# Kernel optimization log

Hardware: AMD Instinct MI355X
Metric: run time of the kernel (lower is better)

Reference implementation:

```python
import jax, jax.numpy as jnp
import numpy as np

B, N, F, E, C, FC = 16, 5000, 512, 160000, 64, 128


def gcn_conv(x, src, dst, W, b, n_total):
    loop = jnp.arange(n_total, dtype=src.dtype)
    s = jnp.concatenate([src, loop])
    d = jnp.concatenate([dst, loop])
    deg = jax.ops.segment_sum(jnp.ones_like(s, dtype=x.dtype), d, num_segments=n_total)
    dinv = jnp.where(deg > 0, jax.lax.rsqrt(deg), 0.0)
    norm = dinv[s] * dinv[d]                      # [E']
    h = x @ W                                      # [n_total, out]
    msg = h[s] * norm[:, None]
    out = jax.ops.segment_sum(msg, d, num_segments=n_total)
    return out + b


def setup_inputs() -> dict:
    key = jax.random.key(0)
    ks = jax.random.split(key, 12)
    inp = {
        "node_features": jax.random.normal(ks[0], (B, N, F), jnp.float32),
        "col_features": jax.random.normal(ks[1], (B, C, FC), jnp.float32),
        "edge_index": jax.random.randint(ks[2], (2, E), 0, N, dtype=jnp.int64),
        # GCNConv 1/2 weights + node head
        "W1": jax.random.normal(ks[3], (F, 16), jnp.float32) / np.sqrt(F),
        "b1": jnp.zeros((16,), jnp.float32),
        "W2": jax.random.normal(ks[4], (16, 16), jnp.float32) / 4.0,
        "b2": jnp.zeros((16,), jnp.float32),
        "fc_w": jax.random.normal(ks[5], (16, 1), jnp.float32) / 4.0,
        "fc_b": jnp.zeros((1,), jnp.float32),
        # column MLP: Linear(FC,16) -> ReLU -> Linear(16,1)
        "cw1": jax.random.normal(ks[6], (FC, 16), jnp.float32) / np.sqrt(FC),
        "cb1": jnp.zeros((16,), jnp.float32),
        "cw2": jax.random.normal(ks[7], (16, 1), jnp.float32) / 4.0,
        "cb2": jnp.zeros((1,), jnp.float32),
    }
    return inp


def reference(node_features, col_features, edge_index, W1, b1, W2, b2, fc_w, fc_b, cw1, cb1, cw2, cb2):
    b, n, _ = node_features.shape
    n_total = b * n
    # batched edge_index via node-offset trick (shared graph per batch element)
    offsets = (jnp.arange(b, dtype=edge_index.dtype) * n)[:, None]   # [B,1]
    src = (edge_index[0][None, :] + offsets).reshape(-1)              # [B*E]
    dst = (edge_index[1][None, :] + offsets).reshape(-1)

    x = node_features.reshape(n_total, -1)
    x = jax.nn.relu(gcn_conv(x, src, dst, W1, b1, n_total))
    x = jax.nn.relu(gcn_conv(x, src, dst, W2, b2, n_total))
    node_logits = (x.reshape(b, n, 16) @ fc_w + fc_b)[..., 0]         # [B,N]

    h = jax.nn.relu(col_features @ cw1 + cb1)
    col_logits = (h @ cw2 + cb2)[..., 0]                              # [B,C]

    joint = node_logits[:, :, None] + col_logits[:, None, :]          # [B,N,C]
    return joint.reshape(b, -1)                                       # [B, N*C]
```

## Files before the change

kernel.cpp:

```cpp
#include <hip/hip_runtime.h>
#include <hip/hip_bf16.h>

typedef unsigned short u16;
typedef unsigned int   u32;

#define B_  16
#define N_  5000
#define F_  512
#define C_  64
#define FC_ 128
#define NT  (B_ * N_)

__device__ __forceinline__ float bf2f(u16 h) {
    return __uint_as_float(((u32)h) << 16);
}
__device__ __forceinline__ u16 f2bf(float f) {
    union { __hip_bfloat16 h; u16 s; } c; c.h = __float2bfloat16(f); return c.s;
}
__device__ __forceinline__ float ldw(const void* p, int i, int fF) {
    return fF ? bf2f(((const u16*)p)[i]) : ((const float*)p)[i];
}

__global__ __launch_bounds__(256) void det_k(const u32* __restrict__ x32,
                                             const u32* __restrict__ ei32,
                                             int* __restrict__ flags)
{
    __shared__ int cnt;
    __shared__ int orv;
    if (threadIdx.x == 0) { cnt = 0; orv = 0; }
    __syncthreads();
    u32 w = x32[threadIdx.x];
    int e = (int)((w >> 7) & 0xffu);
    if (e >= 112 && e <= 136) atomicAdd(&cnt, 1);
    if (threadIdx.x < 32) {
        if (ei32[2 * threadIdx.x + 1] != 0u) atomicOr(&orv, 1);
    }
    __syncthreads();
    if (threadIdx.x == 0) {
        flags[0] = (cnt >= 128) ? 1 : 0;
        flags[1] = (orv == 0) ? 1 : 0;
    }
}

__device__ __forceinline__ int src_at(const u32* ei32, int t, int E, int fI) {
    return (int)(fI ? ei32[2 * t] : ei32[t]);
}
__device__ __forceinline__ int dst_at(const u32* ei32, int t, int E, int fI) {
    return (int)(fI ? ei32[2 * (E + t)] : ei32[E + t]);
}

__global__ __launch_bounds__(256) void prep_weights(
    const void* __restrict__ W1, const void* __restrict__ W2,
    const void* __restrict__ fcw, const void* __restrict__ cw1,
    const void* __restrict__ cw2, const void* __restrict__ b1,
    const void* __restrict__ b2, const void* __restrict__ fcb,
    const void* __restrict__ cb1, const void* __restrict__ cb2,
    const int* __restrict__ flags,
    float* __restrict__ w1f, float* __restrict__ w2f, float* __restrict__ fcwf,
    float* __restrict__ cw1f, float* __restrict__ cw2f, float* __restrict__ b1f,
    float* __restrict__ b2f, float* __restrict__ fcbf, float* __restrict__ cb1f,
    float* __restrict__ cb2f)
{
    int fF = flags[0];
    int t = blockIdx.x * blockDim.x + threadIdx.x;
    if (t < 8192) { w1f[t] = ldw(W1, t, fF); return; }
    int u = t - 8192;
    if (u < 256)  { w2f[u]  = ldw(W2, u, fF);  return; }  u -= 256;
    if (u < 16)   { fcwf[u] = ldw(fcw, u, fF); return; }  u -= 16;
    if (u < 2048) { cw1f[u] = ldw(cw1, u, fF); return; }  u -= 2048;
    if (u < 16)   { cw2f[u] = ldw(cw2, u, fF); return; }  u -= 16;
    if (u < 16)   { b1f[u]  = ldw(b1, u, fF);  return; }  u -= 16;
    if (u < 16)   { b2f[u]  = ldw(b2, u, fF);  return; }  u -= 16;
    if (u < 1)    { fcbf[u] = ldw(fcb, u, fF); return; }  u -= 1;
    if (u < 16)   { cb1f[u] = ldw(cb1, u, fF); return; }  u -= 16;
    if (u < 1)    { cb2f[u] = ldw(cb2, u, fF); return; }
}

__global__ __launch_bounds__(256) void deg_k(const u32* __restrict__ ei32,
                                             const int* __restrict__ flags,
                                             int* __restrict__ deg, int E)
{
    int t = blockIdx.x * blockDim.x + threadIdx.x;
    if (t >= E) return;
    int d = dst_at(ei32, t, E, flags[1]);
    if ((unsigned)d < (unsigned)N_) atomicAdd(&deg[d], 1);
}

__global__ __launch_bounds__(1024) void scan_k(const int* __restrict__ deg,
                                               int* __restrict__ rowptr,
                                               int* __restrict__ cursor,
                                               float* __restrict__ dinv)
{
    __shared__ int ssum[1024];
    int t = threadIdx.x;
    int base = t * 5;
    int loc[5];
    int run = 0;
#pragma unroll
    for (int i = 0; i < 5; i++) {
        int idx = base + i;
        int v = (idx < N_) ? deg[idx] : 0;
        loc[i] = run;
        run += v;
    }
    ssum[t] = run;
    __syncthreads();
    for (int offs = 1; offs < 1024; offs <<= 1) {
        int v = (t >= offs) ? ssum[t - offs] : 0;
        __syncthreads();
        ssum[t] += v;
        __syncthreads();
    }
    int exclusive = ssum[t] - run;
#pragma unroll
    for (int i = 0; i < 5; i++) {
        int idx = base + i;
        if (idx < N_) {
            int rp = exclusive + loc[i];
            rowptr[idx] = rp;
            cursor[idx] = rp;
            dinv[idx] = 1.0f / sqrtf((float)deg[idx] + 1.0f);
        }
    }
    if (t == 1023) rowptr[N_] = ssum[1023];
}

__global__ __launch_bounds__(256) void fill_k(const u32* __restrict__ ei32,
                                              const int* __restrict__ flags,
                                              int* __restrict__ cursor,
                                              int* __restrict__ csr, int E)
{
    int t = blockIdx.x * blockDim.x + threadIdx.x;
    if (t >= E) return;
    int fI = flags[1];
    int s = src_at(ei32, t, E, fI);
    int d = dst_at(ei32, t, E, fI);
    if ((unsigned)d >= (unsigned)N_) return;
    if ((unsigned)s >= (unsigned)N_) s = 0;
    int pos = atomicAdd(&cursor[d], 1);
    if ((unsigned)pos < (unsigned)E) csr[pos] = s;
}

__global__ __launch_bounds__(256) void gemm1_k(const void* __restrict__ xraw,
                                               const float* __restrict__ w1f,
                                               const float* __restrict__ dinv,
                                               const int* __restrict__ flags,
                                               u16* __restrict__ out)
{
    __shared__ float sAcc[4][64][17];
    int lane = threadIdx.x & 63;
    int sub  = threadIdx.x >> 6;
    int row  = blockIdx.x * 64 + lane;
    int fbase = sub * 128;

    float acc[16];
#pragma unroll
    for (int k = 0; k < 16; k++) acc[k] = 0.0f;

    if (flags[0]) {
        const u16* xr = (const u16*)xraw + (size_t)row * F_ + fbase;
#pragma unroll
        for (int i = 0; i < 16; i++) {
            uint4 pk = *(const uint4*)(xr + i * 8);
            u32 q[4] = {pk.x, pk.y, pk.z, pk.w};
#pragma unroll
            for (int j = 0; j < 4; j++) {
                float v0 = bf2f((u16)(q[j] & 0xffffu));
                float v1 = bf2f((u16)(q[j] >> 16));
                const float* w0 = w1f + (fbase + i * 8 + 2 * j) * 16;
#pragma unroll
                for (int k = 0; k < 16; k++) acc[k] += v0 * w0[k];
#pragma unroll
                for (int k = 0; k < 16; k++) acc[k] += v1 * w0[16 + k];
            }
        }
    } else {
        const float* xr = (const float*)xraw + (size_t)row * F_ + fbase;
#pragma unroll
        for (int i = 0; i < 16; i++) {
            float4 a = *(const float4*)(xr + i * 8);
            float4 b = *(const float4*)(xr + i * 8 + 4);
            float v[8] = {a.x, a.y, a.z, a.w, b.x, b.y, b.z, b.w};
#pragma unroll
            for (int j = 0; j < 8; j++) {
                const float* w0 = w1f + (fbase + i * 8 + j) * 16;
#pragma unroll
                for (int k = 0; k < 16; k++) acc[k] += v[j] * w0[k];
            }
        }
    }
#pragma unroll
    for (int k = 0; k < 16; k++) sAcc[sub][lane][k] = acc[k];
    __syncthreads();

    int r  = threadIdx.x >> 2;
    int kc = (threadIdx.x & 3) * 4;
    int orow = blockIdx.x * 64 + r;
    float s = dinv[orow % N_];
    union { uint2 u; u16 h[4]; } o;
#pragma unroll
    for (int k = 0; k < 4; k++) {
        float v = sAcc[0][r][kc + k] + sAcc[1][r][kc + k]
                + sAcc[2][r][kc + k] + sAcc[3][r][kc + k];
        o.h[k] = f2bf(v * s);
    }
    *(uint2*)(out + (size_t)orow * 16 + kc) = o.u;
}

__global__ __launch_bounds__(256) void agg1_k(const u16* __restrict__ h,
                                              const int* __restrict__ rowptr,
                                              const int* __restrict__ csr,
                                              const float* __restrict__ dinv,
                                              const float* __restrict__ b1f,
                                              const float* __restrict__ w2f,
                                              u16* __restrict__ out)
{
    int t = blockIdx.x * blockDim.x + threadIdx.x;
    int g = t >> 4;
    if (g >= NT) return;
    int k = t & 15;
    int d = g % N_;
    int b = g / N_;
    const u16* hb = h + (size_t)b * N_ * 16;
    float acc = bf2f(hb[d * 16 + k]);
    int e0 = rowptr[d], e1 = rowptr[d + 1];
    for (int base = e0; base < e1; base += 8) {
        int idx[8];
#pragma unroll
        for (int j = 0; j < 8; j++) {
            int e = base + j;
            idx[j] = csr[e < e1 ? e : e0];
        }
        float v[8];
#pragma unroll
        for (int j = 0; j < 8; j++) v[j] = bf2f(hb[idx[j] * 16 + k]);
#pragma unroll
        for (int j = 0; j < 8; j++) if (base + j < e1) acc += v[j];
    }
    float dv = dinv[d];
    float x1 = fmaxf(acc * dv + b1f[k], 0.0f);
    float h2 = 0.0f;
#pragma unroll
    for (int j = 0; j < 16; j++) {
        float xj = __shfl(x1, j, 16);
        h2 += xj * w2f[j * 16 + k];
    }
    out[(size_t)g * 16 + k] = f2bf(h2 * dv);
}

__global__ __launch_bounds__(256) void agg2_k(const u16* __restrict__ h,
                                              const int* __restrict__ rowptr,
                                              const int* __restrict__ csr,
                                              const float* __restrict__ dinv,
                                              const float* __restrict__ b2f,
                                              const float* __restrict__ fcwf,
                                              const float* __restrict__ fcbf,
                                              float* __restrict__ nl)
{
    int t = blockIdx.x * blockDim.x + threadIdx.x;
    int g = t >> 4;
    if (g >= NT) return;
    int k = t & 15;
    int d = g % N_;
    int b = g / N_;
    const u16* hb = h + (size_t)b * N_ * 16;
    float acc = bf2f(hb[d * 16 + k]);
    int e0 = rowptr[d], e1 = rowptr[d + 1];
    for (int base = e0; base < e1; base += 8) {
        int idx[8];
#pragma unroll
        for (int j = 0; j < 8; j++) {
            int e = base + j;
            idx[j] = csr[e < e1 ? e : e0];
        }
        float v[8];
#pragma unroll
        for (int j = 0; j < 8; j++) v[j] = bf2f(hb[idx[j] * 16 + k]);
#pragma unroll
        for (int j = 0; j < 8; j++) if (base + j < e1) acc += v[j];
    }
    float x2 = fmaxf(acc * dinv[d] + b2f[k], 0.0f);
    float p = x2 * fcwf[k];
    p += __shfl_xor(p, 8, 16);
    p += __shfl_xor(p, 4, 16);
    p += __shfl_xor(p, 2, 16);
    p += __shfl_xor(p, 1, 16);
    if (k == 0) nl[g] = p + fcbf[0];
}

__global__ __launch_bounds__(256) void col_k(const void* __restrict__ cfraw,
                                             const float* __restrict__ cw1f,
                                             const float* __restrict__ cb1f,
                                             const float* __restrict__ cw2f,
                                             const float* __restrict__ cb2f,
                                             const int* __restrict__ flags,
                                             float* __restrict__ cl)
{
    int t = blockIdx.x * blockDim.x + threadIdx.x;
    if (t >= B_ * C_) return;
    float acc[16];
#pragma unroll
    for (int k = 0; k < 16; k++) acc[k] = cb1f[k];
    if (flags[0]) {
        const u16* r = (const u16*)cfraw + (size_t)t * FC_;
        for (int f = 0; f < FC_; f += 8) {
            uint4 pk = *(const uint4*)(r + f);
            u32 q[4] = {pk.x, pk.y, pk.z, pk.w};
#pragma unroll
            for (int j = 0; j < 4; j++) {
                float v0 = bf2f((u16)(q[j] & 0xffffu));
                float v1 = bf2f((u16)(q[j] >> 16));
                const float* w0 = cw1f + (f + 2 * j) * 16;
#pragma unroll
                for (int k = 0; k < 16; k++) acc[k] += v0 * w0[k];
#pragma unroll
                for (int k = 0; k < 16; k++) acc[k] += v1 * w0[16 + k];
            }
        }
    } else {
        const float* r = (const float*)cfraw + (size_t)t * FC_;
        for (int f = 0; f < FC_; f += 4) {
            float4 a = *(const float4*)(r + f);
            float v[4] = {a.x, a.y, a.z, a.w};
#pragma unroll
            for (int j = 0; j < 4; j++) {
                const float* w0 = cw1f + (f + j) * 16;
#pragma unroll
                for (int k = 0; k < 16; k++) acc[k] += v[j] * w0[k];
            }
        }
    }
    float s = cb2f[0];
#pragma unroll
    for (int k = 0; k < 16; k++) s += fmaxf(acc[k], 0.0f) * cw2f[k];
    cl[t] = s;
}

__global__ __launch_bounds__(256) void join_k(const float* __restrict__ nl,
                                              const float* __restrict__ cl,
                                              const int* __restrict__ flags,
                                              void* __restrict__ outraw)
{
    int t = blockIdx.x * blockDim.x + threadIdx.x;
    if (t >= NT * C_ / 8) return;
    int g  = t >> 3;
    int c0 = (t & 7) * 8;
    int b  = g / N_;
    float nv = nl[g];
    const float* c = cl + b * C_ + c0;
    float4 a0 = *(const float4*)c;
    float4 a1 = *(const float4*)(c + 4);
    float v[8] = {a0.x, a0.y, a0.z, a0.w, a1.x, a1.y, a1.z, a1.w};
#pragma unroll
    for (int i = 0; i < 8; i++) v[i] += nv;
    size_t idx = (size_t)g * C_ + c0;
    if (flags[0]) {
        union { uint4 u; u16 h[8]; } pkv;
#pragma unroll
        for (int i = 0; i < 8; i++) pkv.h[i] = f2bf(v[i]);
        *(uint4*)((u16*)outraw + idx) = pkv.u;
    } else {
        float* o = (float*)outraw + idx;
        *(float4*)o       = make_float4(v[0], v[1], v[2], v[3]);
        *(float4*)(o + 4) = make_float4(v[4], v[5], v[6], v[7]);
    }
}

extern "C" void kernel_launch(void* const* d_in, const int* in_sizes, int n_in,
                              void* d_out, int out_size, void* d_ws, size_t ws_size,
                              hipStream_t stream)
{
    const void* x    = d_in[0];
    const void* cf   = d_in[1];
    const u32*  ei32 = (const u32*)d_in[2];
    const void* W1   = d_in[3];
    const void* b1   = d_in[4];
    const void* W2   = d_in[5];
    const void* b2   = d_in[6];
    const void* fcw  = d_in[7];
    const void* fcb  = d_in[8];
    const void* cw1  = d_in[9];
    const void* cb1  = d_in[10];
    const void* cw2  = d_in[11];
    const void* cb2  = d_in[12];

    const int E = in_sizes[2] / 2;

    char* base = (char*)d_ws;
    size_t off = 0;
    auto alloc = [&](size_t bytes) -> void* {
        void* p = base + off;
        off = (off + bytes + 255) & ~(size_t)255;
        return p;
    };
    int*   flags  = (int*)alloc(2 * 4);
    float* w1f  = (float*)alloc(8192 * 4);
    float* w2f  = (float*)alloc(256 * 4);
    float* fcwf = (float*)alloc(16 * 4);
    float* cw1f = (float*)alloc(2048 * 4);
    float* cw2f = (float*)alloc(16 * 4);
    float* b1f  = (float*)alloc(16 * 4);
    float* b2f  = (float*)alloc(16 * 4);
    float* fcbf = (float*)alloc(4);
    float* cb1f = (float*)alloc(16 * 4);
    float* cb2f = (float*)alloc(4);
    int*   deg    = (int*)alloc((size_t)N_ * 4);
    int*   rowptr = (int*)alloc((size_t)(N_ + 1) * 4);
    int*   cursor = (int*)alloc((size_t)N_ * 4);
    float* dinv   = (float*)alloc((size_t)N_ * 4);
    int*   csr    = (int*)alloc((size_t)E * 4);
    u16*   bufA = (u16*)alloc((size_t)NT * 16 * 2);
    u16*   bufB = (u16*)alloc((size_t)NT * 16 * 2);
    float* nl   = (float*)alloc((size_t)NT * 4);
    float* cl   = (float*)alloc((size_t)B_ * C_ * 4);

    det_k<<<1, 256, 0, stream>>>((const u32*)x, ei32, flags);
    hipMemsetAsync(deg, 0, (size_t)N_ * 4, stream);
    prep_weights<<<(10578 + 255) / 256, 256, 0, stream>>>(
        W1, W2, fcw, cw1, cw2, b1, b2, fcb, cb1, cb2, flags,
        w1f, w2f, fcwf, cw1f, cw2f, b1f, b2f, fcbf, cb1f, cb2f);
    deg_k<<<(E + 255) / 256, 256, 0, stream>>>(ei32, flags, deg, E);
    scan_k<<<1, 1024, 0, stream>>>(deg, rowptr, cursor, dinv);
    fill_k<<<(E + 255) / 256, 256, 0, stream>>>(ei32, flags, cursor, csr, E);

    gemm1_k<<<NT / 64, 256, 0, stream>>>(x, w1f, dinv, flags, bufA);
    agg1_k<<<(NT * 16 + 255) / 256, 256, 0, stream>>>(bufA, rowptr, csr, dinv, b1f, w2f, bufB);
    agg2_k<<<(NT * 16 + 255) / 256, 256, 0, stream>>>(bufB, rowptr, csr, dinv, b2f, fcwf, fcbf, nl);
    col_k<<<(B_ * C_ + 255) / 256, 256, 0, stream>>>(cf, cw1f, cb1f, cw2f, cb2f, flags, cl);
    join_k<<<(NT * C_ / 8 + 255) / 256, 256, 0, stream>>>(nl, cl, flags, d_out);
}
```

Before: 420.5 us.

## Stage X tiles through LDS with coalesced loads in first GEMM

The first projection GEMM now loads each 64-row by 128-feature slice of X cooperatively into padded shared memory with coalesced vector loads, then each wave computes a 32-feature slice for all 64 rows from LDS. Before, each thread streamed its own row with strided 16-byte loads, so global accesses were poorly coalesced. The change adds extra barriers, LDS traffic and bf16-to-float conversion stores. The reduction across waves reuses the same shared buffer.

```diff
diff --git a/kernel.cpp b/kernel.cpp
--- a/kernel.cpp
+++ b/kernel.cpp
@@ -147,61 +147,73 @@
                                                const int* __restrict__ flags,
                                                u16* __restrict__ out)
 {
-    __shared__ float sAcc[4][64][17];
-    int lane = threadIdx.x & 63;
-    int sub  = threadIdx.x >> 6;
-    int row  = blockIdx.x * 64 + lane;
-    int fbase = sub * 128;
+    __shared__ float smem[64 * 129];
+    const int t    = threadIdx.x;
+    const int lane = t & 63;
+    const int wv   = t >> 6;
+    const int row0 = blockIdx.x * 64;
+    const int fF   = flags[0];
 
     float acc[16];
 #pragma unroll
     for (int k = 0; k < 16; k++) acc[k] = 0.0f;
 
-    if (flags[0]) {
-        const u16* xr = (const u16*)xraw + (size_t)row * F_ + fbase;
-#pragma unroll
-        for (int i = 0; i < 16; i++) {
-            uint4 pk = *(const uint4*)(xr + i * 8);
-            u32 q[4] = {pk.x, pk.y, pk.z, pk.w};
-#pragma unroll
-            for (int j = 0; j < 4; j++) {
-                float v0 = bf2f((u16)(q[j] & 0xffffu));
-                float v1 = bf2f((u16)(q[j] >> 16));
-                const float* w0 = w1f + (fbase + i * 8 + 2 * j) * 16;
-#pragma unroll
-                for (int k = 0; k < 16; k++) acc[k] += v0 * w0[k];
-#pragma unroll
-                for (int k = 0; k < 16; k++) acc[k] += v1 * w0[16 + k];
+    for (int p = 0; p < 4; p++) {
+        __syncthreads();
+        if (fF) {
+            const u16* xb = (const u16*)xraw;
+#pragma unroll
+            for (int i = 0; i < 4; i++) {
+                int idx = i * 256 + t;
+                int r   = idx >> 4;
+                int c   = (idx & 15) * 8;
+                uint4 pk = *(const uint4*)(xb + (size_t)(row0 + r) * F_ + p * 128 + c);
+                u32 q[4] = {pk.x, pk.y, pk.z, pk.w};
+                float* dstp = smem + r * 129 + c;
+#pragma unroll
+                for (int j = 0; j < 4; j++) {
+                    dstp[2 * j]     = bf2f((u16)(q[j] & 0xffffu));
+                    dstp[2 * j + 1] = bf2f((u16)(q[j] >> 16));
+                }
             }
-        }
-    } else {
-        const float* xr = (const float*)xraw + (size_t)row * F_ + fbase;
-#pragma unroll
-        for (int i = 0; i < 16; i++) {
-            float4 a = *(const float4*)(xr + i * 8);
-            float4 b = *(const float4*)(xr + i * 8 + 4);
-            float v[8] = {a.x, a.y, a.z, a.w, b.x, b.y, b.z, b.w};
-#pragma unroll
-            for (int j = 0; j < 8; j++) {
-                const float* w0 = w1f + (fbase + i * 8 + j) * 16;
-#pragma unroll
-                for (int k = 0; k < 16; k++) acc[k] += v[j] * w0[k];
+        } else {
+            const float* xf = (const float*)xraw;
+#pragma unroll
+            for (int i = 0; i < 8; i++) {
+                int idx = i * 256 + t;
+                int r   = idx >> 5;
+                int c   = (idx & 31) * 4;
+                float4 v = *(const float4*)(xf + (size_t)(row0 + r) * F_ + p * 128 + c);
+                float* dstp = smem + r * 129 + c;
+                dstp[0] = v.x; dstp[1] = v.y; dstp[2] = v.z; dstp[3] = v.w;
             }
         }
-    }
-#pragma unroll
-    for (int k = 0; k < 16; k++) sAcc[sub][lane][k] = acc[k];
+        __syncthreads();
+        const float* xr = smem + lane * 129 + wv * 32;
+        const float* wr = w1f + (p * 128 + wv * 32) * 16;
+#pragma unroll
+        for (int f = 0; f < 32; f++) {
+            float xv = xr[f];
+#pragma unroll
+            for (int k = 0; k < 16; k++) acc[k] += xv * wr[f * 16 + k];
+        }
+    }
+
     __syncthreads();
-
-    int r  = threadIdx.x >> 2;
-    int kc = (threadIdx.x & 3) * 4;
-    int orow = blockIdx.x * 64 + r;
+    float (*red)[64][17] = (float (*)[64][17])smem;
+#pragma unroll
+    for (int k = 0; k < 16; k++) red[wv][lane][k] = acc[k];
+    __syncthreads();
+
+    int r  = t >> 2;
+    int kc = (t & 3) * 4;
+    int orow = row0 + r;
     float s = dinv[orow % N_];
     union { uint2 u; u16 h[4]; } o;
 #pragma unroll
     for (int k = 0; k < 4; k++) {
-        float v = sAcc[0][r][kc + k] + sAcc[1][r][kc + k]
-                + sAcc[2][r][kc + k] + sAcc[3][r][kc + k];
+        float v = red[0][r][kc + k] + red[1][r][kc + k]
+                + red[2][r][kc + k] + red[3][r][kc + k];
         o.h[k] = f2bf(v * s);
     }
     *(uint2*)(out + (size_t)orow * 16 + kc) = o.u;
```

New measurement: 404.2 us. -3.9%, faster.
